# Performance work log

Measured on AMD Instinct MI355X. Metric: run time of the kernel, lower is better.

The kernel has to match this reference:

```python
import jax, jax.numpy as jnp
import numpy as np

NUM_POINTS = 32
NUM_RESIDUALS = 2
DIST_THRESHOLD = 5.0
H = W = 128
C = 16


def setup_inputs() -> dict:
    key = jax.random.key(0)
    k = jax.random.split(key, 6)
    return {
        "md_maps": jax.random.uniform(k[0], (1, 3, H, W), dtype=jnp.float32),
        "dis_maps": jax.random.uniform(k[1], (1, 1, H, W), dtype=jnp.float32),
        "residual_maps": jax.random.uniform(k[2], (1, 1, H, W), dtype=jnp.float32),
        "features": jax.random.normal(k[3], (C, H, W), dtype=jnp.float32),
        "jloc": jax.random.uniform(k[4], (1, H, W), dtype=jnp.float32),
        "joff": jax.random.uniform(k[5], (2, H, W), dtype=jnp.float32),
        "topk": 300,
    }


def hafm_decoding(md_maps, dis_maps, residual_maps):
    scale = DIST_THRESHOLD
    b, _, h, w = md_maps.shape
    y0, x0 = jnp.meshgrid(jnp.arange(h, dtype=jnp.float32),
                          jnp.arange(w, dtype=jnp.float32), indexing='ij')
    y0 = y0[None, None]
    x0 = x0[None, None]
    sign_pad = jnp.arange(-NUM_RESIDUALS, NUM_RESIDUALS + 1, dtype=jnp.float32).reshape(1, -1, 1, 1)
    dist = jnp.clip(dis_maps + residual_maps * sign_pad, 0.0, 1.0)  # [B, 2R+1, H, W]
    md_un = (md_maps[:, :1] - 0.5) * np.pi * 2.0
    st_un = md_maps[:, 1:2] * np.pi / 2.0
    ed_un = -md_maps[:, 2:3] * np.pi / 2.0
    cs_md = jnp.cos(md_un)
    ss_md = jnp.sin(md_un)
    y_st = jnp.tan(st_un)
    y_ed = jnp.tan(ed_un)
    x_st_final = jnp.clip((cs_md - ss_md * y_st) * dist * scale + x0, 0.0, w - 1)
    y_st_final = jnp.clip((ss_md + cs_md * y_st) * dist * scale + y0, 0.0, h - 1)
    x_ed_final = jnp.clip((cs_md - ss_md * y_ed) * dist * scale + x0, 0.0, w - 1)
    y_ed_final = jnp.clip((ss_md + cs_md * y_ed) * dist * scale + y0, 0.0, h - 1)
    lines = jnp.stack((x_st_final, y_st_final, x_ed_final, y_ed_final), axis=-1)
    return lines.reshape(b, -1, 4)  # [B, (2R+1)*H*W, 4]


def compute_loi_features(features_per_image, lines_per_im, tspan):
    c, h, w = features_per_image.shape
    U, V = lines_per_im[:, :2], lines_per_im[:, 2:]
    pts = U[:, :, None] * tspan + V[:, :, None] * (1.0 - tspan) - 0.5  # [N, 2, P]
    pts = pts.transpose(0, 2, 1).reshape(-1, 2)  # [N*P, 2]
    px, py = pts[:, 0], pts[:, 1]
    px0 = jnp.clip(jnp.floor(px), 0.0, w - 1)
    py0 = jnp.clip(jnp.floor(py), 0.0, h - 1)
    px1 = jnp.clip(px0 + 1.0, 0.0, w - 1)
    py1 = jnp.clip(py0 + 1.0, 0.0, h - 1)
    px0l, py0l = px0.astype(jnp.int32), py0.astype(jnp.int32)
    px1l, py1l = px1.astype(jnp.int32), py1.astype(jnp.int32)
    xp = (features_per_image[:, py0l, px0l] * (py1 - py) * (px1 - px)
          + features_per_image[:, py1l, px0l] * (py - py0) * (px1 - px)
          + features_per_image[:, py0l, px1l] * (py1 - py) * (px - px0)
          + features_per_image[:, py1l, px1l] * (py - py0) * (px - px0))  # [C, N*P]
    xp = xp.reshape(c, -1, tspan.size).transpose(1, 0, 2)  # [N, C, P]
    return xp.reshape(xp.shape[0], -1)  # [N, C*P]


def non_maximum_suppression(a):
    # a: [B, 1, H, W]; torch max_pool2d pads with -inf for max pooling
    ap = jax.lax.reduce_window(a, -jnp.inf, jax.lax.max, (1, 1, 3, 3), (1, 1, 1, 1),
                               [(0, 0), (0, 0), (1, 1), (1, 1)])
    return a * (a == ap).astype(a.dtype)


def get_junctions(jloc, joff, topk):
    h, w = jloc.shape[-2], jloc.shape[-1]
    flat = jloc.reshape(-1)
    joff2 = joff.reshape(2, -1)
    scores, index = jax.lax.top_k(flat, topk)
    y = (index // w).astype(jnp.float32) + joff2[1][index] + 0.5
    x = (index % w).astype(jnp.float32) + joff2[0][index] + 0.5
    junctions = jnp.stack((x, y), axis=1)  # [topk, 2]
    return junctions, scores


def reference(md_maps, dis_maps, residual_maps, features, jloc, joff, topk):
    tspan = jnp.linspace(0.0, 1.0, NUM_POINTS, dtype=jnp.float32)[None, None, :]
    lines = hafm_decoding(md_maps, dis_maps, residual_maps)  # [1, 5*H*W, 4]
    loi = compute_loi_features(features, lines[0], tspan)    # [5*H*W, C*P]
    jloc_nms = non_maximum_suppression(jloc[None])            # [1, 1, H, W]
    junctions, scores = get_junctions(jloc_nms[0], joff, topk)
    return loi, junctions, scores
```

## Files before the change

kernel.cpp:

```cpp
#include <hip/hip_runtime.h>
#include <math.h>

#define HPX 128
#define WPX 128
#define HW  16384
#define CCH 16
#define NLINES 81920
#define NPTS 32
#define LOI_SIZE (NLINES * 512)
#define SORT_N 8192
#define NBINS 4096
#define CAND 1024
#define PREP_TRANS (HW * CCH)

#define FEAT_T_OFF 0
#define LINES_OFF  1048576
#define KEYS_OFF   (1048576 + 1310720)
#define HIST_OFF   (KEYS_OFF + 65536)
#define CTR_OFF    (HIST_OFF + 16384)

__global__ __launch_bounds__(256) void prep_kernel(
        const float* __restrict__ feat, float* __restrict__ feat_t,
        const float* __restrict__ md,
        const float* __restrict__ dis,
        const float* __restrict__ res,
        float4* __restrict__ lines,
        unsigned int* __restrict__ hist,
        unsigned int* __restrict__ ctr) {
    int tid = blockIdx.x * 256 + threadIdx.x;

    if (tid < NBINS) hist[tid] = 0u;
    if (tid == NBINS) ctr[0] = 0u;

    if (tid < PREP_TRANS) {
        int pix = tid >> 4;
        int c   = tid & 15;
        feat_t[tid] = feat[c * HW + pix];
    } else {
        int line = tid - PREP_TRANS;
        int r    = line >> 14;
        int pix  = line & (HW - 1);
        int y0i  = pix >> 7, x0i = pix & 127;

        float md0 = md[pix], md1 = md[HW + pix], md2 = md[2 * HW + pix];
        float dv  = dis[pix], rv = res[pix];

        float dist = fminf(fmaxf(dv + rv * ((float)r - 2.0f), 0.0f), 1.0f);
        float d5   = dist * 5.0f;
        float md_un = (md0 - 0.5f) * 6.28318530717958647692f;
        float cs = cosf(md_un), ss = sinf(md_un);
        float y_st = tanf(md1 * 1.57079632679489661923f);
        float y_ed = tanf(-md2 * 1.57079632679489661923f);

        float x0f = (float)x0i, y0f = (float)y0i;
        float4 ep;
        ep.x = fminf(fmaxf((cs - ss * y_st) * d5 + x0f, 0.0f), 127.0f);
        ep.y = fminf(fmaxf((ss + cs * y_st) * d5 + y0f, 0.0f), 127.0f);
        ep.z = fminf(fmaxf((cs - ss * y_ed) * d5 + x0f, 0.0f), 127.0f);
        ep.w = fminf(fmaxf((ss + cs * y_ed) * d5 + y0f, 0.0f), 127.0f);
        lines[line] = ep;
    }
}

__global__ __launch_bounds__(256) void nms_compact(
        const float* __restrict__ jloc,
        unsigned long long* __restrict__ keys,
        unsigned int* __restrict__ hist,
        unsigned int* __restrict__ ctr) {
    int pix = blockIdx.x * 256 + threadIdx.x;
    if (pix >= HW) return;
    int y = pix >> 7, x = pix & 127;
    float a = jloc[pix];
    float m = a;
    #pragma unroll
    for (int dy = -1; dy <= 1; dy++) {
        #pragma unroll
        for (int dx = -1; dx <= 1; dx++) {
            int yy = y + dy, xx = x + dx;
            if (yy >= 0 && yy < HPX && xx >= 0 && xx < WPX) {
                m = fmaxf(m, jloc[yy * WPX + xx]);
            }
        }
    }
    if (a == m && a > 0.0f) {
        unsigned int slot = atomicAdd(ctr, 1u);
        if (slot < SORT_N) {
            unsigned int bits = __float_as_uint(a);
            keys[slot] = ((unsigned long long)bits << 32)
                       | (unsigned long long)(0xFFFFFFFFu - (unsigned int)pix);
        }
        int bin = min(NBINS - 1, (int)(a * (float)NBINS));
        atomicAdd(&hist[bin], 1u);
    }
}

__global__ __launch_bounds__(1024) void select_topk(
        const unsigned long long* __restrict__ keys_g,
        const unsigned int* __restrict__ ctr,
        const unsigned int* __restrict__ hist,
        const float* __restrict__ joff,
        float* __restrict__ junc, float* __restrict__ scores, int topk) {
    __shared__ unsigned int h[NBINS];
    __shared__ unsigned long long cand[CAND];
    __shared__ unsigned int scount;
    __shared__ int Ts;
    int t = threadIdx.x;

    #pragma unroll
    for (int r = 0; r < 4; r++) h[t + r * 1024] = hist[t + r * 1024];
    if (t == 0) { scount = 0; Ts = 0; }
    __syncthreads();

    for (int off = 1; off < NBINS; off <<= 1) {
        unsigned int v[4];
        #pragma unroll
        for (int r = 0; r < 4; r++) {
            int i = t + r * 1024;
            v[r] = (i + off < NBINS) ? h[i + off] : 0u;
        }
        __syncthreads();
        #pragma unroll
        for (int r = 0; r < 4; r++) h[t + r * 1024] += v[r];
        __syncthreads();
    }

    #pragma unroll
    for (int r = 0; r < 4; r++) {
        int b = t + r * 1024;
        unsigned int sb = h[b];
        unsigned int sn = (b + 1 < NBINS) ? h[b + 1] : 0u;
        if (sb >= (unsigned int)topk && sn < (unsigned int)topk) Ts = b;
    }
    __syncthreads();
    int T = Ts;

    int n = min(ctr[0], (unsigned int)SORT_N);
    for (int i = t; i < n; i += 1024) {
        unsigned long long kk = keys_g[i];
        float val = __uint_as_float((unsigned int)(kk >> 32));
        int bin = min(NBINS - 1, (int)(val * (float)NBINS));
        if (bin >= T) {
            unsigned int p = atomicAdd(&scount, 1u);
            if (p < CAND) cand[p] = kk;
        }
    }
    __syncthreads();
    unsigned int sc = min(scount, (unsigned int)CAND);

    if (t < (int)sc) {
        unsigned long long k = cand[t];
        int r = 0;
        for (unsigned int j = 0; j < sc; j++) r += (cand[j] > k) ? 1 : 0;
        if (r < topk) {
            float val = __uint_as_float((unsigned int)(k >> 32));
            unsigned int idx = 0xFFFFFFFFu - (unsigned int)(k & 0xFFFFFFFFull);
            if (idx >= HW) idx = 0;
            float xo = joff[idx];
            float yo = joff[HW + idx];
            junc[2 * r]     = (float)(idx & 127) + xo + 0.5f;
            junc[2 * r + 1] = (float)(idx >> 7)  + yo + 0.5f;
            scores[r] = val;
        }
    }
    if (t >= (int)sc && t < topk) {
        junc[2 * t]     = joff[0] + 0.5f;
        junc[2 * t + 1] = joff[HW] + 0.5f;
        scores[t] = 0.0f;
    }
}

__global__ __launch_bounds__(256) void loi_kernel(
        const float4* __restrict__ lines,
        const float4* __restrict__ feat4,
        float* __restrict__ out) {
    int tid  = blockIdx.x * 256 + threadIdx.x;
    int cq   = tid & 3;
    int p    = (tid >> 2) & 31;
    int line = tid >> 7;

    float4 ep = lines[line];

    float tk = (float)p * (1.0f / 31.0f);
    float px = ep.x * tk + ep.z * (1.0f - tk) - 0.5f;
    float py = ep.y * tk + ep.w * (1.0f - tk) - 0.5f;

    float px0 = fminf(fmaxf(floorf(px), 0.0f), 127.0f);
    float py0 = fminf(fmaxf(floorf(py), 0.0f), 127.0f);
    float px1 = fminf(px0 + 1.0f, 127.0f);
    float py1 = fminf(py0 + 1.0f, 127.0f);

    float wx1 = px - px0, wx0 = px1 - px;
    float wy1 = py - py0, wy0 = py1 - py;
    float w00 = wy0 * wx0, w01 = wy0 * wx1;
    float w10 = wy1 * wx0, w11 = wy1 * wx1;

    int r0 = ((int)py0) * WPX;
    int r1 = ((int)py1) * WPX;
    int c0 = (int)px0;
    int c1 = (int)px1;

    float4 a = feat4[(r0 + c0) * 4 + cq];
    float4 b = feat4[(r0 + c1) * 4 + cq];
    float4 c = feat4[(r1 + c0) * 4 + cq];
    float4 d = feat4[(r1 + c1) * 4 + cq];

    float v0 = a.x * w00 + b.x * w01 + c.x * w10 + d.x * w11;
    float v1 = a.y * w00 + b.y * w01 + c.y * w10 + d.y * w11;
    float v2 = a.z * w00 + b.z * w01 + c.z * w10 + d.z * w11;
    float v3 = a.w * w00 + b.w * w01 + c.w * w10 + d.w * w11;

    float* ob = out + (size_t)line * 512 + cq * 128 + p;
    __builtin_nontemporal_store(v0, ob);
    __builtin_nontemporal_store(v1, ob + 32);
    __builtin_nontemporal_store(v2, ob + 64);
    __builtin_nontemporal_store(v3, ob + 96);
}

extern "C" void kernel_launch(void* const* d_in, const int* in_sizes, int n_in,
                              void* d_out, int out_size, void* d_ws, size_t ws_size,
                              hipStream_t stream) {
    const float* md   = (const float*)d_in[0];
    const float* dis  = (const float*)d_in[1];
    const float* res  = (const float*)d_in[2];
    const float* feat = (const float*)d_in[3];
    const float* jloc = (const float*)d_in[4];
    const float* joff = (const float*)d_in[5];
    int topk = (out_size - LOI_SIZE) / 3;

    char* ws = (char*)d_ws;
    float* feat_t             = (float*)(ws + FEAT_T_OFF);
    float4* lines             = (float4*)(ws + LINES_OFF);
    unsigned long long* keys  = (unsigned long long*)(ws + KEYS_OFF);
    unsigned int* hist        = (unsigned int*)(ws + HIST_OFF);
    unsigned int* ctr         = (unsigned int*)(ws + CTR_OFF);

    float* out    = (float*)d_out;
    float* junc   = out + LOI_SIZE;
    float* scores = junc + 2 * topk;

    prep_kernel <<<(PREP_TRANS + NLINES) / 256, 256, 0, stream>>>(
                    feat, feat_t, md, dis, res, lines, hist, ctr);
    nms_compact <<<HW / 256, 256, 0, stream>>>(jloc, keys, hist, ctr);
    select_topk <<<1, 1024, 0, stream>>>(keys, ctr, hist, joff, junc, scores, topk);
    loi_kernel  <<<(NLINES * 128) / 256, 256, 0, stream>>>(
                    lines, (const float4*)feat_t, out);
}
```

Before: 218.4 us.

## Fuse NMS into prep kernel and build histogram in select_topk shared memory

Folds the NMS pass into the prep kernel, which now writes a dense per-pixel key array with zero for suppressed pixels, removing one kernel launch and the global atomics on the counter and histogram. The single-block select_topk builds the histogram with shared-memory atomics over all 16384 keys. It then replaces the 12-step barrier-heavy suffix scan with a per-thread 4-bin scan, a wavefront shuffle scan and a cross-wave combine. The cost is that the single block now reads every pixel's key twice instead of only the compacted candidates.

```diff
diff --git a/kernel.cpp b/kernel.cpp
--- a/kernel.cpp
+++ b/kernel.cpp
@@ -8,16 +8,14 @@
 #define NLINES 81920
 #define NPTS 32
 #define LOI_SIZE (NLINES * 512)
-#define SORT_N 8192
 #define NBINS 4096
 #define CAND 1024
 #define PREP_TRANS (HW * CCH)
+#define PREP_TOTAL (PREP_TRANS + NLINES + HW)
 
 #define FEAT_T_OFF 0
 #define LINES_OFF  1048576
 #define KEYS_OFF   (1048576 + 1310720)
-#define HIST_OFF   (KEYS_OFF + 65536)
-#define CTR_OFF    (HIST_OFF + 16384)
 
 __global__ __launch_bounds__(256) void prep_kernel(
         const float* __restrict__ feat, float* __restrict__ feat_t,
@@ -25,18 +23,15 @@
         const float* __restrict__ dis,
         const float* __restrict__ res,
         float4* __restrict__ lines,
-        unsigned int* __restrict__ hist,
-        unsigned int* __restrict__ ctr) {
+        const float* __restrict__ jloc,
+        unsigned long long* __restrict__ keys_full) {
     int tid = blockIdx.x * 256 + threadIdx.x;
-
-    if (tid < NBINS) hist[tid] = 0u;
-    if (tid == NBINS) ctr[0] = 0u;
 
     if (tid < PREP_TRANS) {
         int pix = tid >> 4;
         int c   = tid & 15;
         feat_t[tid] = feat[c * HW + pix];
-    } else {
+    } else if (tid < PREP_TRANS + NLINES) {
         int line = tid - PREP_TRANS;
         int r    = line >> 14;
         int pix  = line & (HW - 1);
@@ -59,89 +54,98 @@
         ep.z = fminf(fmaxf((cs - ss * y_ed) * d5 + x0f, 0.0f), 127.0f);
         ep.w = fminf(fmaxf((ss + cs * y_ed) * d5 + y0f, 0.0f), 127.0f);
         lines[line] = ep;
-    }
-}
-
-__global__ __launch_bounds__(256) void nms_compact(
-        const float* __restrict__ jloc,
-        unsigned long long* __restrict__ keys,
-        unsigned int* __restrict__ hist,
-        unsigned int* __restrict__ ctr) {
-    int pix = blockIdx.x * 256 + threadIdx.x;
-    if (pix >= HW) return;
-    int y = pix >> 7, x = pix & 127;
-    float a = jloc[pix];
-    float m = a;
-    #pragma unroll
-    for (int dy = -1; dy <= 1; dy++) {
+    } else {
+        int pix = tid - PREP_TRANS - NLINES;
+        int y = pix >> 7, x = pix & 127;
+        float a = jloc[pix];
+        float m = a;
         #pragma unroll
-        for (int dx = -1; dx <= 1; dx++) {
-            int yy = y + dy, xx = x + dx;
-            if (yy >= 0 && yy < HPX && xx >= 0 && xx < WPX) {
-                m = fmaxf(m, jloc[yy * WPX + xx]);
+        for (int dy = -1; dy <= 1; dy++) {
+            #pragma unroll
+            for (int dx = -1; dx <= 1; dx++) {
+                int yy = y + dy, xx = x + dx;
+                if (yy >= 0 && yy < HPX && xx >= 0 && xx < WPX) {
+                    m = fmaxf(m, jloc[yy * WPX + xx]);
+                }
             }
         }
-    }
-    if (a == m && a > 0.0f) {
-        unsigned int slot = atomicAdd(ctr, 1u);
-        if (slot < SORT_N) {
-            unsigned int bits = __float_as_uint(a);
-            keys[slot] = ((unsigned long long)bits << 32)
-                       | (unsigned long long)(0xFFFFFFFFu - (unsigned int)pix);
-        }
-        int bin = min(NBINS - 1, (int)(a * (float)NBINS));
-        atomicAdd(&hist[bin], 1u);
+        unsigned long long kk = 0ull;
+        if (a == m && a > 0.0f) {
+            kk = ((unsigned long long)__float_as_uint(a) << 32)
+               | (unsigned long long)(0xFFFFFFFFu - (unsigned int)pix);
+        }
+        keys_full[pix] = kk;
     }
 }
 
 __global__ __launch_bounds__(1024) void select_topk(
-        const unsigned long long* __restrict__ keys_g,
-        const unsigned int* __restrict__ ctr,
-        const unsigned int* __restrict__ hist,
+        const unsigned long long* __restrict__ keys_full,
         const float* __restrict__ joff,
         float* __restrict__ junc, float* __restrict__ scores, int topk) {
     __shared__ unsigned int h[NBINS];
     __shared__ unsigned long long cand[CAND];
+    __shared__ unsigned int wt[16];
+    __shared__ unsigned int wo[16];
     __shared__ unsigned int scount;
     __shared__ int Ts;
     int t = threadIdx.x;
-
-    #pragma unroll
-    for (int r = 0; r < 4; r++) h[t + r * 1024] = hist[t + r * 1024];
+    int l = t & 63, w = t >> 6;
+
+    #pragma unroll
+    for (int r = 0; r < 4; r++) h[t * 4 + r] = 0u;
     if (t == 0) { scount = 0; Ts = 0; }
     __syncthreads();
 
-    for (int off = 1; off < NBINS; off <<= 1) {
-        unsigned int v[4];
-        #pragma unroll
-        for (int r = 0; r < 4; r++) {
-            int i = t + r * 1024;
-            v[r] = (i + off < NBINS) ? h[i + off] : 0u;
-        }
-        __syncthreads();
-        #pragma unroll
-        for (int r = 0; r < 4; r++) h[t + r * 1024] += v[r];
-        __syncthreads();
-    }
-
-    #pragma unroll
-    for (int r = 0; r < 4; r++) {
-        int b = t + r * 1024;
-        unsigned int sb = h[b];
-        unsigned int sn = (b + 1 < NBINS) ? h[b + 1] : 0u;
-        if (sb >= (unsigned int)topk && sn < (unsigned int)topk) Ts = b;
-    }
+    #pragma unroll
+    for (int i = 0; i < 16; i++) {
+        unsigned long long kk = keys_full[t + i * 1024];
+        if (kk) {
+            float val = __uint_as_float((unsigned int)(kk >> 32));
+            int bin = min(NBINS - 1, (int)(val * (float)NBINS));
+            atomicAdd(&h[bin], 1u);
+        }
+    }
+    __syncthreads();
+
+    unsigned int h0 = h[4 * t], h1 = h[4 * t + 1],
+                 h2 = h[4 * t + 2], h3 = h[4 * t + 3];
+    unsigned int s3 = h3, s2 = h2 + s3, s1 = h1 + s2, s0 = h0 + s1;
+
+    unsigned int x = s0;
+    #pragma unroll
+    for (int off = 1; off < 64; off <<= 1) {
+        unsigned int y = __shfl_down(x, off);
+        if (l + off < 64) x += y;
+    }
+    if (l == 0) wt[w] = x;
+    __syncthreads();
+    if (t < 16) {
+        unsigned int acc = 0;
+        for (int ww = 15; ww > t; ww--) acc += wt[ww];
+        wo[t] = acc;
+    }
+    __syncthreads();
+
+    unsigned int A  = wo[w] + (x - s0);
+    unsigned int S0 = s0 + A, S1 = s1 + A, S2 = s2 + A, S3 = s3 + A;
+    unsigned int tku = (unsigned int)topk;
+    if (S0 >= tku && S1 < tku) Ts = 4 * t;
+    if (S1 >= tku && S2 < tku) Ts = 4 * t + 1;
+    if (S2 >= tku && S3 < tku) Ts = 4 * t + 2;
+    if (S3 >= tku && A  < tku) Ts = 4 * t + 3;
     __syncthreads();
     int T = Ts;
 
-    int n = min(ctr[0], (unsigned int)SORT_N);
-    for (int i = t; i < n; i += 1024) {
-        unsigned long long kk = keys_g[i];
-        float val = __uint_as_float((unsigned int)(kk >> 32));
-        int bin = min(NBINS - 1, (int)(val * (float)NBINS));
-        if (bin >= T) {
-            unsigned int p = atomicAdd(&scount, 1u);
-            if (p < CAND) cand[p] = kk;
+    #pragma unroll
+    for (int i = 0; i < 16; i++) {
+        unsigned long long kk = keys_full[t + i * 1024];
+        if (kk) {
+            float val = __uint_as_float((unsigned int)(kk >> 32));
+            int bin = min(NBINS - 1, (int)(val * (float)NBINS));
+            if (bin >= T) {
+                unsigned int p = atomicAdd(&scount, 1u);
+                if (p < CAND) cand[p] = kk;
+            }
         }
     }
     __syncthreads();
@@ -228,20 +232,17 @@
     int topk = (out_size - LOI_SIZE) / 3;
 
     char* ws = (char*)d_ws;
-    float* feat_t             = (float*)(ws + FEAT_T_OFF);
-    float4* lines             = (float4*)(ws + LINES_OFF);
-    unsigned long long* keys  = (unsigned long long*)(ws + KEYS_OFF);
-    unsigned int* hist        = (unsigned int*)(ws + HIST_OFF);
-    unsigned int* ctr         = (unsigned int*)(ws + CTR_OFF);
+    float* feat_t                 = (float*)(ws + FEAT_T_OFF);
+    float4* lines                 = (float4*)(ws + LINES_OFF);
+    unsigned long long* keys_full = (unsigned long long*)(ws + KEYS_OFF);
 
     float* out    = (float*)d_out;
     float* junc   = out + LOI_SIZE;
     float* scores = junc + 2 * topk;
 
-    prep_kernel <<<(PREP_TRANS + NLINES) / 256, 256, 0, stream>>>(
-                    feat, feat_t, md, dis, res, lines, hist, ctr);
-    nms_compact <<<HW / 256, 256, 0, stream>>>(jloc, keys, hist, ctr);
-    select_topk <<<1, 1024, 0, stream>>>(keys, ctr, hist, joff, junc, scores, topk);
+    prep_kernel <<<PREP_TOTAL / 256, 256, 0, stream>>>(
+                    feat, feat_t, md, dis, res, lines, jloc, keys_full);
+    select_topk <<<1, 1024, 0, stream>>>(keys_full, joff, junc, scores, topk);
     loi_kernel  <<<(NLINES * 128) / 256, 256, 0, stream>>>(
                     lines, (const float4*)feat_t, out);
 }
```

Measured after the change: 216.5 us (median of 2 runs). Within noise of the previous version (-0.9%).
